# Optimization experiments

Hardware: AMD Instinct MI355X
Metric: run time of the kernel (lower is better)

Reference implementation:

```python
import jax, jax.numpy as jnp
import numpy as np

EMBED = 768
HEADS = 12
HEAD_DIM = EMBED // HEADS

def setup_inputs() -> dict:
    key = jax.random.key(0)
    k1, k2, k3, k4 = jax.random.split(key, 4)
    x = jax.random.normal(k1, (8, 1024, EMBED), dtype=jnp.float32)
    # qkv Linear (no bias per qkv_bias=False); proj Linear with bias
    w_qkv = jax.random.normal(k2, (EMBED, 3 * EMBED), dtype=jnp.float32) * 0.02
    w_proj = jax.random.normal(k3, (EMBED, EMBED), dtype=jnp.float32) * 0.02
    b_proj = jax.random.normal(k4, (EMBED,), dtype=jnp.float32) * 0.02
    return {"x": x, "w_qkv": w_qkv, "w_proj": w_proj, "b_proj": b_proj}

def reference(x, w_qkv, w_proj, b_proj):
    b, n, e = x.shape
    h, d = HEADS, HEAD_DIM
    scale = d ** (-0.5)
    qkv = x @ w_qkv                                    # [b, n, 3*e]
    qkv = qkv.reshape(b, n, 3, h, d)                   # (qkv h d) split order
    q, k, v = (jnp.transpose(qkv[:, :, i], (0, 2, 1, 3)) for i in range(3))  # [b,h,n,d]
    dots = jnp.einsum('bhid,bhjd->bhij', q, k) * scale
    attn = jax.nn.softmax(dots, axis=-1)               # dropout p=0 -> identity
    out = jnp.einsum('bhij,bhjd->bhid', attn, v)       # [b,h,n,d]
    out = jnp.transpose(out, (0, 2, 1, 3)).reshape(b, n, e)
    return out @ w_proj + b_proj
```

## Files before the change

kernel.cpp:

```cpp
#include <hip/hip_runtime.h>

typedef _Float16 f16;
typedef _Float16 half8 __attribute__((ext_vector_type(8)));
typedef _Float16 half4v __attribute__((ext_vector_type(4)));
typedef __fp16 fp16x2 __attribute__((ext_vector_type(2)));
typedef float f32x4 __attribute__((ext_vector_type(4)));
typedef float f32x16 __attribute__((ext_vector_type(16)));
typedef unsigned uint4v __attribute__((ext_vector_type(4)));

#define MFMA16(a,b,c) __builtin_amdgcn_mfma_f32_16x16x32_f16((a),(b),(c),0,0,0)
#define MFMA32(a,b,c) __builtin_amdgcn_mfma_f32_32x32x16_f16((a),(b),(c),0,0,0)

__device__ __forceinline__ void gload_lds16(const f16* g, f16* l) {
    __builtin_amdgcn_global_load_lds(
        (const __attribute__((address_space(1))) unsigned int*)g,
        (__attribute__((address_space(3))) unsigned int*)l, 16, 0, 0);
}

__device__ __forceinline__ void plswap(unsigned &a, unsigned &b) {
    asm volatile("v_permlane32_swap_b32 %0, %1" : "+v"(a), "+v"(b));
}

__device__ __forceinline__ unsigned pk2(float a, float b) {
    return __builtin_bit_cast(unsigned, __builtin_amdgcn_cvt_pkrtz(a, b));
}

__device__ __forceinline__ float xswap32(float x, int hi) {
    unsigned a = __builtin_bit_cast(unsigned, x), b = a;
    asm volatile("v_permlane32_swap_b32 %0, %1" : "+v"(a), "+v"(b));
    return __builtin_bit_cast(float, hi ? a : b);
}

__global__ void cast_f32_to_f16(const float* __restrict__ in, f16* __restrict__ out, int n4) {
    int i = blockIdx.x * blockDim.x + threadIdx.x;
    if (i < n4) {
        float4 v = ((const float4*)in)[i];
        half4v h;
        h.x = (f16)v.x; h.y = (f16)v.y; h.z = (f16)v.z; h.w = (f16)v.w;
        ((half4v*)out)[i] = h;
    }
}

__global__ void transpose_cast(const float* __restrict__ in, f16* __restrict__ out, int K, int N) {
    __shared__ f16 tile[32][33];
    int n0 = blockIdx.x * 32, k0 = blockIdx.y * 32;
    int tx = threadIdx.x & 31, ty = threadIdx.x >> 5;
    for (int r = ty; r < 32; r += 8)
        tile[r][tx] = (f16)in[(size_t)(k0 + r) * N + (n0 + tx)];
    __syncthreads();
    for (int r = ty; r < 32; r += 8)
        out[(size_t)(n0 + r) * K + (k0 + tx)] = tile[tx][r];
}

template<int MODE>
__global__ __launch_bounds__(256, 3)
void gemm_bt(const f16* __restrict__ A, const f16* __restrict__ Bt,
             f16* __restrict__ qbuf, f16* __restrict__ kbuf, f16* __restrict__ vtbuf,
             float* __restrict__ out, const float* __restrict__ bias)
{
    constexpr int K = 768;
    constexpr int NX = (MODE == 0) ? 18 : 6;
    constexpr int NWG = NX * 64;
    __shared__ __align__(16) char smem[49152];
    f16* As = (f16*)smem;
    f16* Bs = (f16*)(smem + 24576);
    const int tid  = threadIdx.x;
    const int lane = tid & 63, wave = tid >> 6;
    const int wm = wave >> 1, wn = wave & 1;
    const int l15 = lane & 15, l4 = lane >> 4;

    const int bid = blockIdx.x;
    const int swz = (bid & 7) * (NWG / 8) + (bid >> 3);
    const int m0 = (swz / NX) * 128, n0 = (swz % NX) * 128;

    const int srow  = lane >> 2;
    const int sslot = lane & 3;

    f32x4 acc[4][4] = {};

    #define GSTAGE(buf, kt) do {                                                     \
        _Pragma("unroll")                                                            \
        for (int i = 0; i < 2; ++i) {                                                \
            int rbase = i * 64 + wave * 16;                                          \
            int row = rbase + srow;                                                  \
            gload_lds16(A  + (size_t)(m0 + row) * K + (kt) + sslot * 8, &As[(buf) * 4096 + rbase * 32]); \
            gload_lds16(Bt + (size_t)(n0 + row) * K + (kt) + sslot * 8, &Bs[(buf) * 4096 + rbase * 32]); \
        }                                                                            \
    } while (0)

    GSTAGE(0, 0);
    GSTAGE(1, 32);

    int cur = 0;
    for (int t = 0; t < 24; ++t) {
        if (t < 23) asm volatile("s_waitcnt vmcnt(4)" ::: "memory");
        else        asm volatile("s_waitcnt vmcnt(0)" ::: "memory");
        __builtin_amdgcn_s_barrier();
        if (t < 22) {
            int nb = cur + 2; if (nb >= 3) nb -= 3;
            GSTAGE(nb, (t + 2) * 32);
        }
        half8 af[4], bf[4];
        #pragma unroll
        for (int mi = 0; mi < 4; mi++) af[mi] = *(const half8*)&As[cur*4096 + (wm*64 + mi*16 + l15) * 32 + l4*8];
        #pragma unroll
        for (int ni = 0; ni < 4; ni++) bf[ni] = *(const half8*)&Bs[cur*4096 + (wn*64 + ni*16 + l15) * 32 + l4*8];
        #pragma unroll
        for (int mi = 0; mi < 4; mi++)
            #pragma unroll
            for (int ni = 0; ni < 4; ni++)
                acc[mi][ni] = MFMA16(af[mi], bf[ni], acc[mi][ni]);
        if (++cur >= 3) cur = 0;
    }
    #undef GSTAGE

    if (MODE == 0) {
        __syncthreads();
        f16* sC = (f16*)smem;
        const int t3 = n0 / 768;
        const int bb = m0 >> 10;
        const int mo = m0 & 1023;
        const int h0 = (n0 - t3 * 768) >> 6;

        if (t3 < 2) {
            #pragma unroll
            for (int mi = 0; mi < 4; mi++)
                #pragma unroll
                for (int ni = 0; ni < 4; ni++)
                    #pragma unroll
                    for (int r = 0; r < 4; r++) {
                        int row = wm*64 + mi*16 + l4*4 + r;
                        int col = wn*64 + ni*16 + l15;
                        sC[row * 136 + col] = (f16)acc[mi][ni][r];
                    }
            __syncthreads();
            f16* outb = (t3 == 0) ? qbuf : kbuf;
            #pragma unroll
            for (int hc = 0; hc < 2; hc++) {
                f16* base = outb + ((size_t)(bb * 12 + h0 + hc) * 1024 + mo) * 64;
                #pragma unroll
                for (int i = 0; i < 4; i++) {
                    int row = wave * 32 + i * 8 + (lane >> 3);
                    int cc  = (lane & 7) * 8;
                    half8 v = *(const half8*)&sC[row * 136 + hc * 64 + cc];
                    *(half8*)(base + row * 64 + cc) = v;
                }
            }
        } else {
            #pragma unroll
            for (int mi = 0; mi < 4; mi++)
                #pragma unroll
                for (int ni = 0; ni < 4; ni++) {
                    int row0 = wm*64 + mi*16 + l4*4;
                    int col  = wn*64 + ni*16 + l15;
                    half4v pk;
                    #pragma unroll
                    for (int r = 0; r < 4; r++) pk[r] = (f16)acc[mi][ni][r];
                    *(half4v*)&sC[col * 136 + row0] = pk;
                }
            __syncthreads();
            #pragma unroll
            for (int i = 0; i < 8; i++) {
                int col = wave * 32 + i * 4 + (lane >> 4);
                int rc  = (lane & 15) * 8;
                half8 v = *(const half8*)&sC[col * 136 + rc];
                int head = h0 + (col >> 6), dd = col & 63;
                *(half8*)(vtbuf + ((size_t)(bb * 12 + head) * 64 + dd) * 1024 + mo + rc) = v;
            }
        }
    } else {
        #pragma unroll
        for (int mi = 0; mi < 4; mi++)
            #pragma unroll
            for (int ni = 0; ni < 4; ni++)
                #pragma unroll
                for (int r = 0; r < 4; r++) {
                    int gm = m0 + wm*64 + mi*16 + l4*4 + r;
                    int gn = n0 + wn*64 + ni*16 + l15;
                    out[(size_t)gm * 768 + gn] = acc[mi][ni][r] + bias[gn];
                }
    }
}

__global__ __launch_bounds__(256, 4)
void attn_kernel(const f16* __restrict__ qbuf, const f16* __restrict__ kbuf,
                 const f16* __restrict__ vtbuf, f16* __restrict__ obuf)
{
    __shared__ __align__(16) f16 Ks[2][4096];
    __shared__ __align__(16) f16 Vs[2][4096];
    const int tid = threadIdx.x;
    const int lane = tid & 63, wave = tid >> 6;
    const int bh = blockIdx.x;
    const int b = bh / 12, h = bh % 12;
    const int q0 = blockIdx.y * 128 + wave * 32;
    const int l31 = lane & 31, hi = lane >> 5;
    const int sw0 = (l31 & 7) << 4;

    const f16* Q  = qbuf  + (size_t)bh * 65536;
    const f16* Kp = kbuf  + (size_t)bh * 65536;
    const f16* Vt = vtbuf + (size_t)bh * 65536;

    const f16 slh = (f16)(0.125f * 1.44269504089f);
    half8 aq[4];
    #pragma unroll
    for (int c = 0; c < 4; c++) {
        aq[c] = *(const half8*)&Q[(size_t)(q0 + l31) * 64 + c * 16 + hi * 8];
        #pragma unroll
        for (int j = 0; j < 8; j++) aq[c][j] *= slh;
    }

    const int srow8 = lane >> 3;
    const int c16   = (lane & 7) ^ srow8;

    f32x16 o0 = {}, o1 = {};
    float lrq = 0.f, mrq = 0.f;

    #define STAGE(buf, kv) do {                                                     \
        _Pragma("unroll")                                                           \
        for (int i = 0; i < 2; ++i) {                                               \
            int rbase = wave * 16 + i * 8;                                          \
            int rl = rbase + srow8;                                                 \
            gload_lds16(Kp + (size_t)((kv) + rl) * 64 + c16 * 8, &Ks[buf][rbase * 64]); \
            gload_lds16(Vt + (size_t)rl * 1024 + (kv) + c16 * 8, &Vs[buf][rbase * 64]); \
        }                                                                           \
    } while (0)

    STAGE(0, 0);
    __syncthreads();

    for (int t = 0; t < 16; ++t) {
        const int cur = t & 1;
        if (t < 15) STAGE(cur ^ 1, (t + 1) * 64);

        const char* Kb = (const char*)&Ks[cur][0];
        const char* Vb = (const char*)&Vs[cur][0];

        f32x16 st0, st1;
        #pragma unroll
        for (int j = 0; j < 16; j++) { st0[j] = -mrq; st1[j] = -mrq; }
        __builtin_amdgcn_s_setprio(1);
        #pragma unroll
        for (int c = 0; c < 4; c++) {
            int koff = (c * 32 + hi * 16) ^ sw0;
            half8 k0 = *(const half8*)(Kb + l31 * 128 + koff);
            half8 k1 = *(const half8*)(Kb + (32 + l31) * 128 + koff);
            st0 = MFMA32(k0, aq[c], st0);
            st1 = MFMA32(k1, aq[c], st1);
        }
        __builtin_amdgcn_s_setprio(0);

        float m16;
        {
            float p0 = fmaxf(fmaxf(st0[0],  st0[1]),  fmaxf(st0[2],  st0[3]));
            float p1 = fmaxf(fmaxf(st0[4],  st0[5]),  fmaxf(st0[6],  st0[7]));
            float p2 = fmaxf(fmaxf(st0[8],  st0[9]),  fmaxf(st0[10], st0[11]));
            float p3 = fmaxf(fmaxf(st0[12], st0[13]), fmaxf(st0[14], st0[15]));
            float r0 = fmaxf(fmaxf(st1[0],  st1[1]),  fmaxf(st1[2],  st1[3]));
            float r1 = fmaxf(fmaxf(st1[4],  st1[5]),  fmaxf(st1[6],  st1[7]));
            float r2 = fmaxf(fmaxf(st1[8],  st1[9]),  fmaxf(st1[10], st1[11]));
            float r3 = fmaxf(fmaxf(st1[12], st1[13]), fmaxf(st1[14], st1[15]));
            m16 = fmaxf(fmaxf(fmaxf(p0, p1), fmaxf(p2, p3)),
                        fmaxf(fmaxf(r0, r1), fmaxf(r2, r3)));
        }
        m16 = fmaxf(m16, xswap32(m16, hi));

        if (!__all(m16 <= 11.0f)) {
            float d = fmaxf(m16, 0.f);
            float alpha = exp2f(-d);
            mrq += d;
            #pragma unroll
            for (int j = 0; j < 16; j++) { st0[j] -= d; st1[j] -= d; }
            lrq *= alpha;
            #pragma unroll
            for (int reg = 0; reg < 16; reg++) {
                float a = __shfl(alpha, (reg & 3) + 8 * (reg >> 2) + 4 * hi);
                o0[reg] *= a; o1[reg] *= a;
            }
        }

        float rs = 0.f;
        half8 pa[4];
        #pragma unroll
        for (int tile = 0; tile < 2; tile++) {
            const f32x16& sv = tile ? st1 : st0;
            #pragma unroll
            for (int half16 = 0; half16 < 2; half16++) {
                int rb = half16 * 8;
                unsigned A1, B1, A2, B2;
                {
                    float e0 = exp2f(sv[rb+0]), e1 = exp2f(sv[rb+1]);
                    float e4 = exp2f(sv[rb+4]), e5 = exp2f(sv[rb+5]);
                    rs += (e0 + e1) + (e4 + e5);
                    A1 = pk2(e0, e1); B1 = pk2(e4, e5);
                    plswap(A1, B1);
                }
                {
                    float e2 = exp2f(sv[rb+2]), e3 = exp2f(sv[rb+3]);
                    float e6 = exp2f(sv[rb+6]), e7 = exp2f(sv[rb+7]);
                    rs += (e2 + e3) + (e6 + e7);
                    A2 = pk2(e2, e3); B2 = pk2(e6, e7);
                    plswap(A2, B2);
                }
                uint4v w = {A1, A2, B1, B2};
                pa[tile * 2 + half16] = __builtin_bit_cast(half8, w);
            }
        }
        rs += xswap32(rs, hi);
        lrq += rs;

        __builtin_amdgcn_s_setprio(1);
        #pragma unroll
        for (int kc = 0; kc < 4; kc++) {
            int koff = (kc * 32 + hi * 16) ^ sw0;
            half8 v0 = *(const half8*)(Vb + l31 * 128 + koff);
            half8 v1 = *(const half8*)(Vb + (32 + l31) * 128 + koff);
            o0 = MFMA32(pa[kc], v0, o0);
            o1 = MFMA32(pa[kc], v1, o1);
        }
        __builtin_amdgcn_s_setprio(0);

        __syncthreads();
    }
    #undef STAGE

    float rq = 1.0f / lrq;
    f16* Op = obuf + (size_t)b * 1024 * 768 + h * 64;
    #pragma unroll
    for (int reg = 0; reg < 16; reg++) {
        int qrow = (reg & 3) + 8 * (reg >> 2) + 4 * hi;
        float inv = __shfl(rq, qrow);
        size_t base = (size_t)(q0 + qrow) * 768;
        Op[base + l31]      = (f16)(o0[reg] * inv);
        Op[base + 32 + l31] = (f16)(o1[reg] * inv);
    }
}

extern "C" void kernel_launch(void* const* d_in, const int* in_sizes, int n_in,
                              void* d_out, int out_size, void* d_ws, size_t ws_size,
                              hipStream_t stream) {
    const float* x      = (const float*)d_in[0];
    const float* w_qkv  = (const float*)d_in[1];
    const float* w_proj = (const float*)d_in[2];
    const float* b_proj = (const float*)d_in[3];
    float* out = (float*)d_out;
    char* ws = (char*)d_ws;

    f16* x_h      = (f16*)(ws + 0);
    f16* w_qkv_t  = (f16*)(ws + 12582912);
    f16* w_proj_t = (f16*)(ws + 16121856);
    f16* qb       = (f16*)(ws + 17301504);
    f16* kb       = (f16*)(ws + 29884416);
    f16* vtb      = (f16*)(ws + 42467328);
    f16* ob       = (f16*)(ws + 55050240);

    cast_f32_to_f16<<<dim3(6144), dim3(256), 0, stream>>>(x, x_h, 6291456 / 4);
    transpose_cast<<<dim3(2304 / 32, 768 / 32), dim3(256), 0, stream>>>(w_qkv, w_qkv_t, 768, 2304);
    transpose_cast<<<dim3(768 / 32, 768 / 32), dim3(256), 0, stream>>>(w_proj, w_proj_t, 768, 768);
    gemm_bt<0><<<dim3(18 * 64), dim3(256), 0, stream>>>(
        x_h, w_qkv_t, qb, kb, vtb, nullptr, nullptr);
    attn_kernel<<<dim3(96, 8), dim3(256), 0, stream>>>(qb, kb, vtb, ob);
    gemm_bt<1><<<dim3(6 * 64), dim3(256), 0, stream>>>(
        ob, w_proj_t, nullptr, nullptr, nullptr, out, b_proj);
}
```

Baseline: 128.3 us.

## Triple-buffer K/V and software-pipeline next tile's QK^T MFMAs under softmax

The attention kernel moves from double to triple LDS buffering, prefetching K/V two tiles ahead. It issues the QK^T MFMAs for the next tile before the softmax of the current tile, so exp work can overlap matrix-core work. A stale max-shift correction fixes scores computed with an outdated running max. It also switches exp2f to the raw hardware exp2 builtin and lowers the launch-bounds occupancy hint from 4 to 3 blocks, which adds LDS use and register pressure.

New measurement: 121.1 us. 1.06x faster.

```diff
diff --git a/kernel.cpp b/kernel.cpp
--- a/kernel.cpp
+++ b/kernel.cpp
@@ -23,6 +23,14 @@
 
 __device__ __forceinline__ unsigned pk2(float a, float b) {
     return __builtin_bit_cast(unsigned, __builtin_amdgcn_cvt_pkrtz(a, b));
+}
+
+__device__ __forceinline__ float fexp2(float x) {
+#if __has_builtin(__builtin_amdgcn_exp2f)
+    return __builtin_amdgcn_exp2f(x);
+#else
+    return exp2f(x);
+#endif
 }
 
 __device__ __forceinline__ float xswap32(float x, int hi) {
@@ -182,12 +190,12 @@
     }
 }
 
-__global__ __launch_bounds__(256, 4)
+__global__ __launch_bounds__(256, 3)
 void attn_kernel(const f16* __restrict__ qbuf, const f16* __restrict__ kbuf,
                  const f16* __restrict__ vtbuf, f16* __restrict__ obuf)
 {
-    __shared__ __align__(16) f16 Ks[2][4096];
-    __shared__ __align__(16) f16 Vs[2][4096];
+    __shared__ __align__(16) f16 Ks[3][4096];
+    __shared__ __align__(16) f16 Vs[3][4096];
     const int tid = threadIdx.x;
     const int lane = tid & 63, wave = tid >> 6;
     const int bh = blockIdx.x;
@@ -213,7 +221,7 @@
     const int c16   = (lane & 7) ^ srow8;
 
     f32x16 o0 = {}, o1 = {};
-    float lrq = 0.f, mrq = 0.f;
+    float lrq = 0.f, mrq = 0.f, stale = 0.f;
 
     #define STAGE(buf, kv) do {                                                     \
         _Pragma("unroll")                                                           \
@@ -225,29 +233,43 @@
         }                                                                           \
     } while (0)
 
+    #define QKISSUE(dst0, dst1, kb, minit) do {                                     \
+        _Pragma("unroll")                                                           \
+        for (int j = 0; j < 16; j++) { dst0[j] = (minit); dst1[j] = (minit); }      \
+        __builtin_amdgcn_s_setprio(1);                                              \
+        _Pragma("unroll")                                                           \
+        for (int c = 0; c < 4; c++) {                                               \
+            int koff = (c * 32 + hi * 16) ^ sw0;                                    \
+            half8 k0 = *(const half8*)((kb) + l31 * 128 + koff);                    \
+            half8 k1 = *(const half8*)((kb) + (32 + l31) * 128 + koff);             \
+            dst0 = MFMA32(k0, aq[c], dst0);                                         \
+            dst1 = MFMA32(k1, aq[c], dst1);                                         \
+        }                                                                           \
+        __builtin_amdgcn_s_setprio(0);                                              \
+    } while (0)
+
     STAGE(0, 0);
+    STAGE(1, 64);
     __syncthreads();
 
+    f32x16 st0, st1;
+    QKISSUE(st0, st1, (const char*)&Ks[0][0], 0.f);
+
+    int bcur = 0;
     for (int t = 0; t < 16; ++t) {
-        const int cur = t & 1;
-        if (t < 15) STAGE(cur ^ 1, (t + 1) * 64);
-
-        const char* Kb = (const char*)&Ks[cur][0];
-        const char* Vb = (const char*)&Vs[cur][0];
-
-        f32x16 st0, st1;
-        #pragma unroll
-        for (int j = 0; j < 16; j++) { st0[j] = -mrq; st1[j] = -mrq; }
-        __builtin_amdgcn_s_setprio(1);
-        #pragma unroll
-        for (int c = 0; c < 4; c++) {
-            int koff = (c * 32 + hi * 16) ^ sw0;
-            half8 k0 = *(const half8*)(Kb + l31 * 128 + koff);
-            half8 k1 = *(const half8*)(Kb + (32 + l31) * 128 + koff);
-            st0 = MFMA32(k0, aq[c], st0);
-            st1 = MFMA32(k1, aq[c], st1);
-        }
-        __builtin_amdgcn_s_setprio(0);
+        int bn1 = bcur + 1; if (bn1 >= 3) bn1 -= 3;
+        int bn2 = bcur + 2; if (bn2 >= 3) bn2 -= 3;
+
+        if (t < 14) STAGE(bn2, (t + 2) * 64);
+
+        f32x16 sN0, sN1;
+        if (t < 15) QKISSUE(sN0, sN1, (const char*)&Ks[bn1][0], -mrq);
+
+        if (__any(stale != 0.f)) {
+            #pragma unroll
+            for (int j = 0; j < 16; j++) { st0[j] -= stale; st1[j] -= stale; }
+        }
+        stale = 0.f;
 
         float m16;
         {
@@ -266,8 +288,9 @@
 
         if (!__all(m16 <= 11.0f)) {
             float d = fmaxf(m16, 0.f);
-            float alpha = exp2f(-d);
+            float alpha = fexp2(-d);
             mrq += d;
+            stale = d;
             #pragma unroll
             for (int j = 0; j < 16; j++) { st0[j] -= d; st1[j] -= d; }
             lrq *= alpha;
@@ -288,15 +311,15 @@
                 int rb = half16 * 8;
                 unsigned A1, B1, A2, B2;
                 {
-                    float e0 = exp2f(sv[rb+0]), e1 = exp2f(sv[rb+1]);
-                    float e4 = exp2f(sv[rb+4]), e5 = exp2f(sv[rb+5]);
+                    float e0 = fexp2(sv[rb+0]), e1 = fexp2(sv[rb+1]);
+                    float e4 = fexp2(sv[rb+4]), e5 = fexp2(sv[rb+5]);
                     rs += (e0 + e1) + (e4 + e5);
                     A1 = pk2(e0, e1); B1 = pk2(e4, e5);
                     plswap(A1, B1);
                 }
                 {
-                    float e2 = exp2f(sv[rb+2]), e3 = exp2f(sv[rb+3]);
-                    float e6 = exp2f(sv[rb+6]), e7 = exp2f(sv[rb+7]);
+                    float e2 = fexp2(sv[rb+2]), e3 = fexp2(sv[rb+3]);
+                    float e6 = fexp2(sv[rb+6]), e7 = fexp2(sv[rb+7]);
                     rs += (e2 + e3) + (e6 + e7);
                     A2 = pk2(e2, e3); B2 = pk2(e6, e7);
                     plswap(A2, B2);
@@ -308,19 +331,28 @@
         rs += xswap32(rs, hi);
         lrq += rs;
 
-        __builtin_amdgcn_s_setprio(1);
-        #pragma unroll
-        for (int kc = 0; kc < 4; kc++) {
-            int koff = (kc * 32 + hi * 16) ^ sw0;
-            half8 v0 = *(const half8*)(Vb + l31 * 128 + koff);
-            half8 v1 = *(const half8*)(Vb + (32 + l31) * 128 + koff);
-            o0 = MFMA32(pa[kc], v0, o0);
-            o1 = MFMA32(pa[kc], v1, o1);
-        }
-        __builtin_amdgcn_s_setprio(0);
-
-        __syncthreads();
-    }
+        {
+            const char* Vb = (const char*)&Vs[bcur][0];
+            __builtin_amdgcn_s_setprio(1);
+            #pragma unroll
+            for (int kc = 0; kc < 4; kc++) {
+                int koff = (kc * 32 + hi * 16) ^ sw0;
+                half8 v0 = *(const half8*)(Vb + l31 * 128 + koff);
+                half8 v1 = *(const half8*)(Vb + (32 + l31) * 128 + koff);
+                o0 = MFMA32(pa[kc], v0, o0);
+                o1 = MFMA32(pa[kc], v1, o1);
+            }
+            __builtin_amdgcn_s_setprio(0);
+        }
+
+        if (t < 15) {
+            asm volatile("s_waitcnt vmcnt(0)" ::: "memory");
+            __builtin_amdgcn_s_barrier();
+            st0 = sN0; st1 = sN1;
+        }
+        bcur = bn1;
+    }
+    #undef QKISSUE
     #undef STAGE
 
     float rq = 1.0f / lrq;
```
